# Kernel optimization log

Hardware: AMD Instinct MI355X
Metric: run time of the kernel (lower is better)

Reference implementation:

```python
import jax, jax.numpy as jnp
import numpy as np

N_NODES = 50000


def setup_inputs() -> dict:
    key = jax.random.key(0)
    ks = jax.random.split(key, 9)
    B, N, E, IN = 4, N_NODES, 800000, 32
    x = jax.random.normal(ks[0], (B, N, IN), dtype=jnp.float32)
    edge_index = jax.random.randint(ks[1], (2, E), 0, N, dtype=jnp.int64)
    edge_attr = jax.random.normal(ks[2], (E, 1), dtype=jnp.float32)
    W1 = jax.random.normal(ks[3], (2 * IN + 1, 32), dtype=jnp.float32) * 0.1
    b1 = jax.random.normal(ks[4], (32,), dtype=jnp.float32) * 0.1
    W2 = jax.random.normal(ks[5], (32, 30), dtype=jnp.float32) * 0.1
    b2 = jax.random.normal(ks[6], (30,), dtype=jnp.float32) * 0.1
    W3 = jax.random.normal(ks[7], (30, 32), dtype=jnp.float32) * 0.1
    b3 = jax.random.normal(ks[8], (32,), dtype=jnp.float32) * 0.1
    return {"x": x, "edge_index": edge_index, "edge_attr": edge_attr,
            "W1": W1, "b1": b1, "W2": W2, "b2": b2, "W3": W3, "b3": b3}


def reference(x, edge_index, edge_attr, W1, b1, W2, b2, W3, b3):
    B, N, _ = x.shape
    src, tgt = edge_index[0], edge_index[1]
    # normalize edge attributes over edges (torch .std uses ddof=1)
    ea = (edge_attr - edge_attr.mean(axis=0)) / edge_attr.std(axis=0, ddof=1)
    node_src = x[:, src]      # [B, E, in]
    node_tgt = x[:, tgt]      # [B, E, in]
    ea_b = jnp.broadcast_to(ea[None], (B,) + ea.shape)
    h = jnp.concatenate([node_src, node_tgt, ea_b], axis=-1)  # [B, E, 2*in+1]
    h = jax.nn.sigmoid(h @ W1 + b1)
    h = jax.nn.sigmoid(h @ W2 + b2)   # [B, E, 30]
    seg = lambda vals, idx: jax.ops.segment_sum(vals, idx, num_segments=N)
    out_add = jax.vmap(seg, in_axes=(0, None))(h, tgt)    # [B, N, 30]
    out_sub = jax.vmap(seg, in_axes=(0, None))(-h, src)   # [B, N, 30]
    out = out_add + out_sub
    return jax.nn.sigmoid(out @ W3 + b3)  # [B, N, out_dim]
```

## Files before the change

kernel.cpp:

```cpp
#include <hip/hip_runtime.h>
#include <math.h>

#define B_SZ 4
#define IN_F 32
#define H1_F 32
#define H2_F 30
#define TPW 16
#define HREP 16

typedef unsigned int uint;
typedef unsigned short ushort;
typedef __attribute__((ext_vector_type(8))) short bf16x8;
typedef __attribute__((ext_vector_type(4))) float f32x4;

__device__ __forceinline__ float fastrcp(float x) {
#if __has_builtin(__builtin_amdgcn_rcpf)
    return __builtin_amdgcn_rcpf(x);
#else
    return 1.f / x;
#endif
}
__device__ __forceinline__ float sigmoidf_(float x) {
    return fastrcp(1.f + __expf(-x));
}

__device__ __forceinline__ ushort f2bf(float f) {
    uint u = __float_as_uint(f);
    return (ushort)((u + 0x7FFFu + ((u >> 16) & 1u)) >> 16);
}
__device__ __forceinline__ float bf2f(ushort v) { return __uint_as_float(((uint)v) << 16); }
__device__ __forceinline__ uint pk2(float a, float b) {
    return (uint)f2bf(a) | ((uint)f2bf(b) << 16);
}

union Frag { bf16x8 v; ushort us[8]; uint u[4]; };

__global__ void __launch_bounds__(256) stats_xcvt_kernel(
    const float* __restrict__ ea, const int* __restrict__ ei,
    const float* __restrict__ x, float2* __restrict__ psums,
    int* __restrict__ cnt, ushort* __restrict__ xb,
    int E, int N, long long n8) {
    long long i = (long long)blockIdx.x * 256 + threadIdx.x;
    if (i < n8) {
        const float4* p = (const float4*)(x + i * 8);
        float4 v0 = p[0], v1 = p[1];
        uint4 o;
        o.x = pk2(v0.x, v0.y); o.y = pk2(v0.z, v0.w);
        o.z = pk2(v1.x, v1.y); o.w = pk2(v1.z, v1.w);
        *(uint4*)(xb + i * 8) = o;
    }
    int e = blockIdx.x * 256 + threadIdx.x;
    int* myc = cnt + (size_t)(blockIdx.x & (HREP - 1)) * N;
    float a = (e < E) ? ea[e] : 0.f;
    if (e < E) {
        atomicAdd(&myc[ei[E + e]], 1);
        atomicAdd(&myc[ei[e]], 1);
    }
    float v = a, v2 = a * a;
    for (int off = 32; off > 0; off >>= 1) {
        v  += __shfl_down(v, off);
        v2 += __shfl_down(v2, off);
    }
    __shared__ float s1[4], s2[4];
    int wid = threadIdx.x >> 6, lane = threadIdx.x & 63;
    if (lane == 0) { s1[wid] = v; s2[wid] = v2; }
    __syncthreads();
    if (threadIdx.x == 0) {
        float2 p;
        p.x = s1[0] + s1[1] + s1[2] + s1[3];
        p.y = s2[0] + s2[1] + s2[2] + s2[3];
        psums[blockIdx.x] = p;
    }
}

__global__ void __launch_bounds__(256) sums_reduce_kernel(
    const float2* __restrict__ psums, float* __restrict__ sums, int nblk) {
    float v = 0.f, v2 = 0.f;
    for (int i = threadIdx.x; i < nblk; i += 256) {
        float2 p = psums[i];
        v += p.x; v2 += p.y;
    }
    for (int off = 32; off > 0; off >>= 1) {
        v  += __shfl_down(v, off);
        v2 += __shfl_down(v2, off);
    }
    __shared__ float s1[4], s2[4];
    int wid = threadIdx.x >> 6, lane = threadIdx.x & 63;
    if (lane == 0) { s1[wid] = v; s2[wid] = v2; }
    __syncthreads();
    if (threadIdx.x == 0) {
        sums[0] = s1[0] + s1[1] + s1[2] + s1[3];
        sums[1] = s2[0] + s2[1] + s2[2] + s2[3];
    }
}

__global__ void __launch_bounds__(256) scan1_kernel(const int* __restrict__ cnt,
                                                    int* __restrict__ offs,
                                                    int* __restrict__ bsum, int n) {
    __shared__ int wtot[4];
    int base = blockIdx.x * 1024 + threadIdx.x * 4;
    int4 v = {0, 0, 0, 0};
    if (base + 3 < n) {
#pragma unroll
        for (int r = 0; r < HREP; r++) {
            int4 t = *(const int4*)(cnt + (size_t)r * n + base);
            v.x += t.x; v.y += t.y; v.z += t.z; v.w += t.w;
        }
    } else {
        for (int r = 0; r < HREP; r++) {
            const int* c = cnt + (size_t)r * n;
            if (base < n)     v.x += c[base];
            if (base + 1 < n) v.y += c[base + 1];
            if (base + 2 < n) v.z += c[base + 2];
            if (base + 3 < n) v.w += c[base + 3];
        }
    }
    int s = v.x + v.y + v.z + v.w;
    int incl = s;
    int lane = threadIdx.x & 63;
    for (int d = 1; d < 64; d <<= 1) {
        int t = __shfl_up(incl, d);
        if (lane >= d) incl += t;
    }
    int wid = threadIdx.x >> 6;
    if (lane == 63) wtot[wid] = incl;
    __syncthreads();
    int woff = 0, tot = 0;
#pragma unroll
    for (int w = 0; w < 4; w++) {
        int t = wtot[w];
        if (w < wid) woff += t;
        tot += t;
    }
    int excl = woff + incl - s;
    int4 o;
    o.x = excl; o.y = excl + v.x; o.z = o.y + v.y; o.w = o.z + v.z;
    if (base + 3 < n) *(int4*)(offs + base) = o;
    else {
        if (base < n)     offs[base] = o.x;
        if (base + 1 < n) offs[base + 1] = o.y;
        if (base + 2 < n) offs[base + 2] = o.z;
        if (base + 3 < n) offs[base + 3] = o.w;
    }
    if (threadIdx.x == 0) bsum[blockIdx.x] = tot;
}

__global__ void scan2_kernel(int* __restrict__ bsum, int* __restrict__ offs,
                             int nb, int n) {
    int lane = threadIdx.x;
    if (nb <= 64) {
        int v = (lane < nb) ? bsum[lane] : 0;
        int incl = v;
        for (int d = 1; d < 64; d <<= 1) {
            int t = __shfl_up(incl, d);
            if (lane >= d) incl += t;
        }
        if (lane < nb) bsum[lane] = incl - v;
        if (lane == 63) offs[n] = incl;
    } else if (lane == 0) {
        int run = 0;
        for (int i = 0; i < nb; i++) { int t = bsum[i]; bsum[i] = run; run += t; }
        offs[n] = run;
    }
}

__global__ void __launch_bounds__(256) scan3_kernel(int* __restrict__ offs,
                                                    int* __restrict__ cursor,
                                                    const int* __restrict__ bsum, int n) {
    int base = blockIdx.x * 1024 + threadIdx.x * 4;
    int add = bsum[blockIdx.x];
    if (base + 3 < n) {
        int4 v = *(const int4*)(offs + base);
        v.x += add; v.y += add; v.z += add; v.w += add;
        *(int4*)(offs + base) = v;
        *(int4*)(cursor + base) = v;
    } else {
        for (int k = 0; k < 4; k++) {
            int i = base + k;
            if (i < n) { int v = offs[i] + add; offs[i] = v; cursor[i] = v; }
        }
    }
}

__global__ void __launch_bounds__(256) edge_mlp_e4(
    const ushort* __restrict__ xb,
    const int* __restrict__ ei, const float* __restrict__ ea,
    const float* __restrict__ W1, const float* __restrict__ b1,
    const float* __restrict__ W2, const float* __restrict__ b2,
    const float* __restrict__ sums, int* __restrict__ cursor,
    int* __restrict__ list, ushort* __restrict__ h,
    int E, int N, int tiles) {
    __shared__ ushort __attribute__((aligned(16))) hbuf[4][16 * 40];
    int w = threadIdx.x >> 6;
    int lane = threadIdx.x & 63;
    int n16 = lane & 15;
    int q = lane >> 4;

    Frag w1f[2][2];
#pragma unroll
    for (int t = 0; t < 2; t++)
#pragma unroll
        for (int s = 0; s < 2; s++)
#pragma unroll
            for (int j = 0; j < 4; j++) {
                int k0 = 32 * s + q * 8 + 2 * j;
                w1f[t][s].u[j] = pk2(W1[(size_t)k0 * 32 + 16 * t + n16],
                                     W1[(size_t)(k0 + 1) * 32 + 16 * t + n16]);
            }
    Frag w2f[2];
#pragma unroll
    for (int t = 0; t < 2; t++) {
        int m = 16 * t + n16;
#pragma unroll
        for (int j = 0; j < 4; j++) {
            int k0 = q * 8 + 2 * j;
            float a = (m < H2_F) ? W2[(size_t)k0 * H2_F + m] : 0.f;
            float d = (m < H2_F) ? W2[(size_t)(k0 + 1) * H2_F + m] : 0.f;
            w2f[t].u[j] = pk2(a, d);
        }
    }
    float b1q[2][4], w1Lq[2][4], b2q[2][4];
#pragma unroll
    for (int t = 0; t < 2; t++)
#pragma unroll
        for (int r = 0; r < 4; r++) {
            int col = 16 * t + q * 4 + r;
            b1q[t][r]  = b1[col];
            w1Lq[t][r] = W1[(size_t)64 * 32 + col];
            b2q[t][r]  = (col < H2_F) ? b2[col] : 0.f;
        }

    float mean = sums[0] / (float)E;
    float var = (sums[1] - (float)E * mean * mean) / (float)(E - 1);
    float istd = rsqrtf(var);

    int b  = n16 & 3;
    int el = n16 >> 2;
    int gw = blockIdx.x * 4 + w;
    int tile0 = gw * TPW;
    if (tile0 >= tiles) return;

    int src, tgt; float eav; bool vrow; Frag a0, a1;
    {
        int eA = tile0 * 4 + el; vrow = eA < E; int c = vrow ? eA : E - 1;
        src = ei[c]; tgt = ei[E + c]; eav = (ea[c] - mean) * istd;
        *(uint4*)&a0.u[0] = *(const uint4*)(xb + ((size_t)b * N + src) * IN_F + q * 8);
        *(uint4*)&a1.u[0] = *(const uint4*)(xb + ((size_t)b * N + tgt) * IN_F + q * 8);
        if (lane < 8) {
            int eS = tile0 * 4 + (lane >> 1);
            if (eS < E) {
                int node = (lane & 1) ? ei[eS] : ei[E + eS];
                int s = atomicAdd(&cursor[node], 1);
                list[s] = eS | (int)(((uint)(lane & 1)) << 31);
            }
        }
    }

    for (int tix = 0; tix < TPW; ++tix) {
        int tile = tile0 + tix;
        if (tile >= tiles) break;

        int nsrc = 0, ntgt = 0; float neav = 0.f; bool nvrow = false;
        Frag na0, na1;
        na0.u[0] = na0.u[1] = na0.u[2] = na0.u[3] = 0; na1 = na0;
        bool hn = (tix + 1 < TPW) && (tile + 1 < tiles);
        if (hn) {
            int eA = (tile + 1) * 4 + el; nvrow = eA < E; int c = nvrow ? eA : E - 1;
            nsrc = ei[c]; ntgt = ei[E + c]; neav = (ea[c] - mean) * istd;
            *(uint4*)&na0.u[0] = *(const uint4*)(xb + ((size_t)b * N + nsrc) * IN_F + q * 8);
            *(uint4*)&na1.u[0] = *(const uint4*)(xb + ((size_t)b * N + ntgt) * IN_F + q * 8);
            if (lane < 8) {
                int eS = (tile + 1) * 4 + (lane >> 1);
                if (eS < E) {
                    int node = (lane & 1) ? ei[eS] : ei[E + eS];
                    int s = atomicAdd(&cursor[node], 1);
                    list[s] = eS | (int)(((uint)(lane & 1)) << 31);
                }
            }
        }

        f32x4 acc0, acc1;
#pragma unroll
        for (int r = 0; r < 4; r++) {
            acc0[r] = b1q[0][r] + eav * w1Lq[0][r];
            acc1[r] = b1q[1][r] + eav * w1Lq[1][r];
        }
        acc0 = __builtin_amdgcn_mfma_f32_16x16x32_bf16(w1f[0][0].v, a0.v, acc0, 0, 0, 0);
        acc0 = __builtin_amdgcn_mfma_f32_16x16x32_bf16(w1f[0][1].v, a1.v, acc0, 0, 0, 0);
        acc1 = __builtin_amdgcn_mfma_f32_16x16x32_bf16(w1f[1][0].v, a0.v, acc1, 0, 0, 0);
        acc1 = __builtin_amdgcn_mfma_f32_16x16x32_bf16(w1f[1][1].v, a1.v, acc1, 0, 0, 0);

        uint u0 = pk2(sigmoidf_(acc0[0]), sigmoidf_(acc0[1]));
        uint u1 = pk2(sigmoidf_(acc0[2]), sigmoidf_(acc0[3]));
        uint u2 = pk2(sigmoidf_(acc1[0]), sigmoidf_(acc1[1]));
        uint u3 = pk2(sigmoidf_(acc1[2]), sigmoidf_(acc1[3]));
        uint2 p01 = {u0, u1}, p23 = {u2, u3};
        *(uint2*)&hbuf[w][n16 * 40 + q * 4]      = p01;
        *(uint2*)&hbuf[w][n16 * 40 + 16 + q * 4] = p23;

        Frag ha;
        *(uint4*)&ha.u[0] = *(const uint4*)&hbuf[w][n16 * 40 + q * 8];

        f32x4 c0, c1;
#pragma unroll
        for (int r = 0; r < 4; r++) { c0[r] = b2q[0][r]; c1[r] = b2q[1][r]; }
        c0 = __builtin_amdgcn_mfma_f32_16x16x32_bf16(w2f[0].v, ha.v, c0, 0, 0, 0);
        c1 = __builtin_amdgcn_mfma_f32_16x16x32_bf16(w2f[1].v, ha.v, c1, 0, 0, 0);

        uint g0 = pk2(sigmoidf_(c0[0]), sigmoidf_(c0[1]));
        uint g1 = pk2(sigmoidf_(c0[2]), sigmoidf_(c0[3]));
        uint g2 = pk2(sigmoidf_(c1[0]), sigmoidf_(c1[1]));
        uint g3 = pk2(sigmoidf_(c1[2]), sigmoidf_(c1[3]));

        if (vrow) {
            uint* bt = (uint*)h + (size_t)(tile * 4 + el) * 64 + b * 16;
            uint2 t01; t01.x = g0; t01.y = g1;
            uint2 t23; t23.x = g2; t23.y = g3;
            *(uint2*)(bt + q * 2)     = t01;
            *(uint2*)(bt + 8 + q * 2) = t23;
        }

        src = nsrc; tgt = ntgt; eav = neav; vrow = nvrow;
        a0 = na0; a1 = na1;
    }
}

__global__ void __launch_bounds__(256) gather_e4(
    const ushort* __restrict__ h, const int* __restrict__ list,
    const int* __restrict__ offs, const float* __restrict__ W3,
    const float* __restrict__ b3, float* __restrict__ out, int N) {
    __shared__ float sW3[H2_F * 32];
    __shared__ float sb3[32];
    __shared__ float sacc[4][B_SZ][H2_F];
    for (int i = threadIdx.x; i < H2_F * 32; i += 256) sW3[i] = W3[i];
    if (threadIdx.x < 32) sb3[threadIdx.x] = b3[threadIdx.x];
    __syncthreads();

    int w = threadIdx.x >> 6, lane = threadIdx.x & 63;
    int n = blockIdx.x * 4 + w;
    if (n >= N) return;

    int s = offs[n], e = offs[n + 1];
    int r = (lane < 60) ? lane : 0;
    int bq = r / 15, jp = r % 15;
    const uint* h32 = (const uint*)h;
    float a0 = 0.f, a1 = 0.f;
    int i = (lane < 60) ? s : e;
    for (; i + 3 < e; i += 4) {
        int v0 = list[i], v1 = list[i + 1], v2 = list[i + 2], v3 = list[i + 3];
        uint d0 = h32[(size_t)(v0 & 0x7FFFFFFF) * 64 + bq * 16 + jp];
        uint d1 = h32[(size_t)(v1 & 0x7FFFFFFF) * 64 + bq * 16 + jp];
        uint d2 = h32[(size_t)(v2 & 0x7FFFFFFF) * 64 + bq * 16 + jp];
        uint d3 = h32[(size_t)(v3 & 0x7FFFFFFF) * 64 + bq * 16 + jp];
        float g0 = (v0 < 0) ? -1.f : 1.f;
        float g1 = (v1 < 0) ? -1.f : 1.f;
        float g2 = (v2 < 0) ? -1.f : 1.f;
        float g3 = (v3 < 0) ? -1.f : 1.f;
        a0 += g0 * bf2f((ushort)d0) + g1 * bf2f((ushort)d1)
            + g2 * bf2f((ushort)d2) + g3 * bf2f((ushort)d3);
        a1 += g0 * bf2f((ushort)(d0 >> 16)) + g1 * bf2f((ushort)(d1 >> 16))
            + g2 * bf2f((ushort)(d2 >> 16)) + g3 * bf2f((ushort)(d3 >> 16));
    }
    for (; i < e; i++) {
        int v = list[i];
        uint d = h32[(size_t)(v & 0x7FFFFFFF) * 64 + bq * 16 + jp];
        float g = (v < 0) ? -1.f : 1.f;
        a0 += g * bf2f((ushort)d);
        a1 += g * bf2f((ushort)(d >> 16));
    }
    if (lane < 60) {
        sacc[w][bq][jp * 2]     = a0;
        sacc[w][bq][jp * 2 + 1] = a1;
    }
    int b = lane >> 4, k = lane & 15;
    float o0 = sb3[k], o1 = sb3[k + 16];
#pragma unroll
    for (int j = 0; j < H2_F; j++) {
        float v = sacc[w][b][j];
        o0 += v * sW3[j * 32 + k];
        o1 += v * sW3[j * 32 + k + 16];
    }
    float* op = out + ((size_t)b * N + n) * 32;
    op[k]      = sigmoidf_(o0);
    op[k + 16] = sigmoidf_(o1);
}

__global__ void __launch_bounds__(256) scatter_kernel(const int* __restrict__ ei,
                                                      int* __restrict__ cursor,
                                                      int* __restrict__ list, int E, int N) {
    int e = blockIdx.x * 256 + threadIdx.x;
    if (e < E) {
        int tgt = ei[E + e];
        int p = atomicAdd(&cursor[tgt], 1);
        list[p] = e;
        int src = ei[e];
        int q = atomicAdd(&cursor[src], 1);
        list[q] = e | (int)0x80000000u;
    }
}

template<bool USE_XB>
__global__ void __launch_bounds__(256) edge_mlp_mfma2(
    const float* __restrict__ x, const ushort* __restrict__ xb,
    const int* __restrict__ ei, const float* __restrict__ ea,
    const float* __restrict__ W1, const float* __restrict__ b1,
    const float* __restrict__ W2, const float* __restrict__ b2,
    const float* __restrict__ sums, ushort* __restrict__ h,
    int E, int N, int tiles) {
    __shared__ ushort __attribute__((aligned(16))) hbuf[4][16 * 40];
    int w = threadIdx.x >> 6;
    int lane = threadIdx.x & 63;
    int n16 = lane & 15;
    int q = lane >> 4;

    Frag w1f[2][2];
#pragma unroll
    for (int t = 0; t < 2; t++)
#pragma unroll
        for (int s = 0; s < 2; s++)
#pragma unroll
            for (int j = 0; j < 4; j++) {
                int k0 = 32 * s + q * 8 + 2 * j;
                w1f[t][s].u[j] = pk2(W1[(size_t)k0 * 32 + 16 * t + n16],
                                     W1[(size_t)(k0 + 1) * 32 + 16 * t + n16]);
            }
    Frag w2f[2];
#pragma unroll
    for (int t = 0; t < 2; t++) {
        int m = 16 * t + n16;
#pragma unroll
        for (int j = 0; j < 4; j++) {
            int k0 = q * 8 + 2 * j;
            float a = (m < H2_F) ? W2[(size_t)k0 * H2_F + m] : 0.f;
            float d = (m < H2_F) ? W2[(size_t)(k0 + 1) * H2_F + m] : 0.f;
            w2f[t].u[j] = pk2(a, d);
        }
    }
    float b1q[2][4], w1Lq[2][4], b2q[2][4];
#pragma unroll
    for (int t = 0; t < 2; t++)
#pragma unroll
        for (int r = 0; r < 4; r++) {
            int col = 16 * t + q * 4 + r;
            b1q[t][r]  = b1[col];
            w1Lq[t][r] = W1[(size_t)64 * 32 + col];
            b2q[t][r]  = (col < H2_F) ? b2[col] : 0.f;
        }

    float mean = sums[0] / (float)E;
    float var = (sums[1] - (float)E * mean * mean) / (float)(E - 1);
    float istd = rsqrtf(var);

    int b = n16 & 3;
    int eoff = n16 >> 2;
    int gw = blockIdx.x * 4 + w;

    for (int tix = 0; tix < TPW; ++tix) {
        int tile = gw * TPW + tix;
        if (tile >= tiles) break;
        int e0 = tile * 4;
        int eA = e0 + eoff;
        bool vrow = eA < E;
        int eAc = vrow ? eA : E - 1;
        int src = ei[eAc], tgt = ei[E + eAc];
        float eav = (ea[eAc] - mean) * istd;

        Frag a0, a1;
        if (USE_XB) {
            *(uint4*)&a0.u[0] = *(const uint4*)(xb + ((size_t)b * N + src) * IN_F + q * 8);
            *(uint4*)&a1.u[0] = *(const uint4*)(xb + ((size_t)b * N + tgt) * IN_F + q * 8);
        } else {
            const float4* ps = (const float4*)(x + ((size_t)b * N + src) * IN_F + q * 8);
            float4 s0 = ps[0], s1 = ps[1];
            const float4* pt = (const float4*)(x + ((size_t)b * N + tgt) * IN_F + q * 8);
            float4 t0 = pt[0], t1 = pt[1];
            a0.u[0] = pk2(s0.x, s0.y); a0.u[1] = pk2(s0.z, s0.w);
            a0.u[2] = pk2(s1.x, s1.y); a0.u[3] = pk2(s1.z, s1.w);
            a1.u[0] = pk2(t0.x, t0.y); a1.u[1] = pk2(t0.z, t0.w);
            a1.u[2] = pk2(t1.x, t1.y); a1.u[3] = pk2(t1.z, t1.w);
        }

        f32x4 acc0, acc1;
#pragma unroll
        for (int r = 0; r < 4; r++) {
            acc0[r] = b1q[0][r] + eav * w1Lq[0][r];
            acc1[r] = b1q[1][r] + eav * w1Lq[1][r];
        }
        acc0 = __builtin_amdgcn_mfma_f32_16x16x32_bf16(w1f[0][0].v, a0.v, acc0, 0, 0, 0);
        acc0 = __builtin_amdgcn_mfma_f32_16x16x32_bf16(w1f[0][1].v, a1.v, acc0, 0, 0, 0);
        acc1 = __builtin_amdgcn_mfma_f32_16x16x32_bf16(w1f[1][0].v, a0.v, acc1, 0, 0, 0);
        acc1 = __builtin_amdgcn_mfma_f32_16x16x32_bf16(w1f[1][1].v, a1.v, acc1, 0, 0, 0);

        uint u0 = pk2(sigmoidf_(acc0[0]), sigmoidf_(acc0[1]));
        uint u1 = pk2(sigmoidf_(acc0[2]), sigmoidf_(acc0[3]));
        uint u2 = pk2(sigmoidf_(acc1[0]), sigmoidf_(acc1[1]));
        uint u3 = pk2(sigmoidf_(acc1[2]), sigmoidf_(acc1[3]));
        uint2 p01 = {u0, u1}, p23 = {u2, u3};
        *(uint2*)&hbuf[w][n16 * 40 + q * 4]      = p01;
        *(uint2*)&hbuf[w][n16 * 40 + 16 + q * 4] = p23;

        Frag ha;
        *(uint4*)&ha.u[0] = *(const uint4*)&hbuf[w][n16 * 40 + q * 8];

        f32x4 c0, c1;
#pragma unroll
        for (int r = 0; r < 4; r++) { c0[r] = b2q[0][r]; c1[r] = b2q[1][r]; }
        c0 = __builtin_amdgcn_mfma_f32_16x16x32_bf16(w2f[0].v, ha.v, c0, 0, 0, 0);
        c1 = __builtin_amdgcn_mfma_f32_16x16x32_bf16(w2f[1].v, ha.v, c1, 0, 0, 0);

        uint g0 = pk2(sigmoidf_(c0[0]), sigmoidf_(c0[1]));
        uint g1 = pk2(sigmoidf_(c0[2]), sigmoidf_(c0[3]));
        uint g2 = pk2(sigmoidf_(c1[0]), sigmoidf_(c1[1]));
        uint g3 = pk2(sigmoidf_(c1[2]), sigmoidf_(c1[3]));
        if (vrow) {
            uint* base = (uint*)(h + (size_t)(e0 * 4 + n16) * H2_F);
            base[q * 2]     = g0;
            base[q * 2 + 1] = g1;
            base[8 + q * 2] = g2;
            if (q < 3) base[8 + q * 2 + 1] = g3;
        }
    }
}

__global__ void __launch_bounds__(256) gather_final(
    const ushort* __restrict__ h, const int* __restrict__ list,
    const int* __restrict__ offs, const float* __restrict__ W3,
    const float* __restrict__ b3, float* __restrict__ out, int N) {
    __shared__ float sW3[H2_F * 32];
    __shared__ float sb3[32];
    __shared__ float sacc[4][B_SZ][H2_F];
    for (int i = threadIdx.x; i < H2_F * 32; i += 256) sW3[i] = W3[i];
    if (threadIdx.x < 32) sb3[threadIdx.x] = b3[threadIdx.x];
    __syncthreads();

    int w = threadIdx.x >> 6, lane = threadIdx.x & 63;
    int n = blockIdx.x * 4 + w;
    if (n >= N) return;

    if (lane < 60) {
        int bq = lane / 15, jp = lane % 15;
        float a0 = 0.f, a1 = 0.f;
        int s = offs[n], e = offs[n + 1];
        int i = s;
        for (; i + 4 <= e; i += 4) {
            int v0 = list[i], v1 = list[i + 1], v2 = list[i + 2], v3 = list[i + 3];
            uint d0 = *(const uint*)(h + (size_t)(v0 & 0x7FFFFFFF) * 120 + bq * 30 + jp * 2);
            uint d1 = *(const uint*)(h + (size_t)(v1 & 0x7FFFFFFF) * 120 + bq * 30 + jp * 2);
            uint d2 = *(const uint*)(h + (size_t)(v2 & 0x7FFFFFFF) * 120 + bq * 30 + jp * 2);
            uint d3 = *(const uint*)(h + (size_t)(v3 & 0x7FFFFFFF) * 120 + bq * 30 + jp * 2);
            float g0 = (v0 < 0) ? -1.f : 1.f;
            float g1 = (v1 < 0) ? -1.f : 1.f;
            float g2 = (v2 < 0) ? -1.f : 1.f;
            float g3 = (v3 < 0) ? -1.f : 1.f;
            a0 += g0 * bf2f((ushort)d0) + g1 * bf2f((ushort)d1)
                + g2 * bf2f((ushort)d2) + g3 * bf2f((ushort)d3);
            a1 += g0 * bf2f((ushort)(d0 >> 16)) + g1 * bf2f((ushort)(d1 >> 16))
                + g2 * bf2f((ushort)(d2 >> 16)) + g3 * bf2f((ushort)(d3 >> 16));
        }
        for (; i < e; i++) {
            int v = list[i];
            uint d = *(const uint*)(h + (size_t)(v & 0x7FFFFFFF) * 120 + bq * 30 + jp * 2);
            float g = (v < 0) ? -1.f : 1.f;
            a0 += g * bf2f((ushort)d);
            a1 += g * bf2f((ushort)(d >> 16));
        }
        sacc[w][bq][jp * 2]     = a0;
        sacc[w][bq][jp * 2 + 1] = a1;
    }
    int b = lane >> 4, k = lane & 15;
    float o0 = sb3[k], o1 = sb3[k + 16];
#pragma unroll
    for (int j = 0; j < H2_F; j++) {
        float v = sacc[w][b][j];
        o0 += v * sW3[j * 32 + k];
        o1 += v * sW3[j * 32 + k + 16];
    }
    float* op = out + ((size_t)b * N + n) * 32;
    op[k]      = sigmoidf_(o0);
    op[k + 16] = sigmoidf_(o1);
}

extern "C" void kernel_launch(void* const* d_in, const int* in_sizes, int n_in,
                              void* d_out, int out_size, void* d_ws, size_t ws_size,
                              hipStream_t stream) {
    const float* x  = (const float*)d_in[0];
    const int*   ei = (const int*)d_in[1];
    const float* ea = (const float*)d_in[2];
    const float* W1 = (const float*)d_in[3];
    const float* b1 = (const float*)d_in[4];
    const float* W2 = (const float*)d_in[5];
    const float* b2 = (const float*)d_in[6];
    const float* W3 = (const float*)d_in[7];
    const float* b3 = (const float*)d_in[8];
    float* out = (float*)d_out;

    const int E  = in_sizes[2];
    const int N  = in_sizes[0] / (B_SZ * IN_F);
    const int BN = B_SZ * N;
    const int nb = (N + 1023) / 1024;
    const long long n8 = (long long)BN * IN_F / 8;
    const int nblkC = (int)(((long long)E > n8 ? (long long)E : n8) + 255) / 256;

    char* base = (char*)d_ws;

    size_t off = 0;
    int* cnt    = (int*)(base + off); off += (size_t)HREP * N * 4;
    float* sums = (float*)(base + off); off += 8;
    int* offs   = (int*)(base + off); off += (size_t)(N + 1) * 4;
    int* cursor = (int*)(base + off); off += (size_t)N * 4;
    int* bsum   = (int*)(base + off); off += 4096;
    off = (off + 255) & ~(size_t)255;
    float2* psums = (float2*)(base + off); off += (size_t)nblkC * 8;
    off = (off + 255) & ~(size_t)255;
    int* list   = (int*)(base + off); off += (size_t)2 * E * 4;
    off = (off + 255) & ~(size_t)255;
    ushort* h   = (ushort*)(base + off); off += (size_t)E * 256;
    off = (off + 255) & ~(size_t)255;
    ushort* xb  = (ushort*)(base + off); off += (size_t)BN * IN_F * 2;
    size_t needA = off;

    size_t offB = 0;
    int* cntB    = (int*)(base + offB); offB += (size_t)HREP * N * 4;
    float* sumsB = (float*)(base + offB); offB += 8;
    int* offsB   = (int*)(base + offB); offB += (size_t)(N + 1) * 4;
    int* cursorB = (int*)(base + offB); offB += (size_t)N * 4;
    int* bsumB   = (int*)(base + offB); offB += 4096;
    offB = (offB + 255) & ~(size_t)255;
    float2* psumsB = (float2*)(base + offB); offB += (size_t)nblkC * 8;
    int* listB   = (int*)(base + offB); offB += (size_t)2 * E * 4;
    offB = (offB + 255) & ~(size_t)255;
    ushort* hB   = (ushort*)(base + offB); offB += (size_t)E * 240;
    offB = (offB + 255) & ~(size_t)255;
    ushort* xbB  = (ushort*)(base + offB);
    size_t needB = offB + (size_t)BN * IN_F * 2;

    if (ws_size >= needA) {
        const int tiles = (E + 3) / 4;
        const int waves = (tiles + TPW - 1) / TPW;
        const int eblocks = (waves + 3) / 4;
        hipMemsetAsync(cnt, 0, (size_t)HREP * N * 4 + 8, stream);
        stats_xcvt_kernel<<<nblkC, 256, 0, stream>>>(ea, ei, x, psums, cnt, xb, E, N, n8);
        sums_reduce_kernel<<<1, 256, 0, stream>>>(psums, sums, nblkC);
        scan1_kernel<<<nb, 256, 0, stream>>>(cnt, offs, bsum, N);
        scan2_kernel<<<1, 64, 0, stream>>>(bsum, offs, nb, N);
        scan3_kernel<<<nb, 256, 0, stream>>>(offs, cursor, bsum, N);
        edge_mlp_e4<<<eblocks, 256, 0, stream>>>(xb, ei, ea, W1, b1, W2, b2,
                                                 sums, cursor, list, h, E, N, tiles);
        gather_e4<<<(N + 3) / 4, 256, 0, stream>>>(h, list, offs, W3, b3, out, N);
    } else {
        const int tiles = (E + 3) / 4;
        const int waves = (tiles + TPW - 1) / TPW;
        const int eblocks = (waves + 3) / 4;
        bool use_xb = (ws_size >= needB);
        hipMemsetAsync(cntB, 0, (size_t)HREP * N * 4 + 8, stream);
        stats_xcvt_kernel<<<nblkC, 256, 0, stream>>>(ea, ei, x, psumsB, cntB,
                                                     use_xb ? xbB : (ushort*)nullptr,
                                                     E, N, use_xb ? n8 : 0LL);
        sums_reduce_kernel<<<1, 256, 0, stream>>>(psumsB, sumsB, nblkC);
        scan1_kernel<<<nb, 256, 0, stream>>>(cntB, offsB, bsumB, N);
        scan2_kernel<<<1, 64, 0, stream>>>(bsumB, offsB, nb, N);
        scan3_kernel<<<nb, 256, 0, stream>>>(offsB, cursorB, bsumB, N);
        scatter_kernel<<<(E + 255) / 256, 256, 0, stream>>>(ei, cursorB, listB, E, N);
        if (use_xb)
            edge_mlp_mfma2<true><<<eblocks, 256, 0, stream>>>(x, xbB, ei, ea, W1, b1,
                                                              W2, b2, sumsB, hB, E, N, tiles);
        else
            edge_mlp_mfma2<false><<<eblocks, 256, 0, stream>>>(x, xbB, ei, ea, W1, b1,
                                                               W2, b2, sumsB, hB, E, N, tiles);
        gather_final<<<(N + 3) / 4, 256, 0, stream>>>(hB, listB, offsB, W3, b3, out, N);
    }
}
```

Baseline: 438.3 us.

## Use hardware bf16 pack, nontemporal list stores, and 8-way gather unroll

```diff
diff --git a/kernel.cpp b/kernel.cpp
--- a/kernel.cpp
+++ b/kernel.cpp
@@ -10,6 +10,7 @@
 
 typedef unsigned int uint;
 typedef unsigned short ushort;
+typedef unsigned long long ull;
 typedef __attribute__((ext_vector_type(8))) short bf16x8;
 typedef __attribute__((ext_vector_type(4))) float f32x4;
 
@@ -31,6 +32,11 @@
 __device__ __forceinline__ float bf2f(ushort v) { return __uint_as_float(((uint)v) << 16); }
 __device__ __forceinline__ uint pk2(float a, float b) {
     return (uint)f2bf(a) | ((uint)f2bf(b) << 16);
+}
+__device__ __forceinline__ uint pk2f(float a, float b) {
+    uint r;
+    asm("v_cvt_pk_bf16_f32 %0, %1, %2" : "=v"(r) : "v"(a), "v"(b));
+    return r;
 }
 
 union Frag { bf16x8 v; ushort us[8]; uint u[4]; };
@@ -45,8 +51,8 @@
         const float4* p = (const float4*)(x + i * 8);
         float4 v0 = p[0], v1 = p[1];
         uint4 o;
-        o.x = pk2(v0.x, v0.y); o.y = pk2(v0.z, v0.w);
-        o.z = pk2(v1.x, v1.y); o.w = pk2(v1.z, v1.w);
+        o.x = pk2f(v0.x, v0.y); o.y = pk2f(v0.z, v0.w);
+        o.z = pk2f(v1.x, v1.y); o.w = pk2f(v1.z, v1.w);
         *(uint4*)(xb + i * 8) = o;
     }
     int e = blockIdx.x * 256 + threadIdx.x;
@@ -251,7 +257,7 @@
             if (eS < E) {
                 int node = (lane & 1) ? ei[eS] : ei[E + eS];
                 int s = atomicAdd(&cursor[node], 1);
-                list[s] = eS | (int)(((uint)(lane & 1)) << 31);
+                __builtin_nontemporal_store(eS | (int)(((uint)(lane & 1)) << 31), &list[s]);
             }
         }
     }
@@ -274,7 +280,7 @@
                 if (eS < E) {
                     int node = (lane & 1) ? ei[eS] : ei[E + eS];
                     int s = atomicAdd(&cursor[node], 1);
-                    list[s] = eS | (int)(((uint)(lane & 1)) << 31);
+                    __builtin_nontemporal_store(eS | (int)(((uint)(lane & 1)) << 31), &list[s]);
                 }
             }
         }
@@ -290,10 +296,10 @@
         acc1 = __builtin_amdgcn_mfma_f32_16x16x32_bf16(w1f[1][0].v, a0.v, acc1, 0, 0, 0);
         acc1 = __builtin_amdgcn_mfma_f32_16x16x32_bf16(w1f[1][1].v, a1.v, acc1, 0, 0, 0);
 
-        uint u0 = pk2(sigmoidf_(acc0[0]), sigmoidf_(acc0[1]));
-        uint u1 = pk2(sigmoidf_(acc0[2]), sigmoidf_(acc0[3]));
-        uint u2 = pk2(sigmoidf_(acc1[0]), sigmoidf_(acc1[1]));
-        uint u3 = pk2(sigmoidf_(acc1[2]), sigmoidf_(acc1[3]));
+        uint u0 = pk2f(sigmoidf_(acc0[0]), sigmoidf_(acc0[1]));
+        uint u1 = pk2f(sigmoidf_(acc0[2]), sigmoidf_(acc0[3]));
+        uint u2 = pk2f(sigmoidf_(acc1[0]), sigmoidf_(acc1[1]));
+        uint u3 = pk2f(sigmoidf_(acc1[2]), sigmoidf_(acc1[3]));
         uint2 p01 = {u0, u1}, p23 = {u2, u3};
         *(uint2*)&hbuf[w][n16 * 40 + q * 4]      = p01;
         *(uint2*)&hbuf[w][n16 * 40 + 16 + q * 4] = p23;
@@ -307,10 +313,10 @@
         c0 = __builtin_amdgcn_mfma_f32_16x16x32_bf16(w2f[0].v, ha.v, c0, 0, 0, 0);
         c1 = __builtin_amdgcn_mfma_f32_16x16x32_bf16(w2f[1].v, ha.v, c1, 0, 0, 0);
 
-        uint g0 = pk2(sigmoidf_(c0[0]), sigmoidf_(c0[1]));
-        uint g1 = pk2(sigmoidf_(c0[2]), sigmoidf_(c0[3]));
-        uint g2 = pk2(sigmoidf_(c1[0]), sigmoidf_(c1[1]));
-        uint g3 = pk2(sigmoidf_(c1[2]), sigmoidf_(c1[3]));
+        uint g0 = pk2f(sigmoidf_(c0[0]), sigmoidf_(c0[1]));
+        uint g1 = pk2f(sigmoidf_(c0[2]), sigmoidf_(c0[3]));
+        uint g2 = pk2f(sigmoidf_(c1[0]), sigmoidf_(c1[1]));
+        uint g3 = pk2f(sigmoidf_(c1[2]), sigmoidf_(c1[3]));
 
         if (vrow) {
             uint* bt = (uint*)h + (size_t)(tile * 4 + el) * 64 + b * 16;
@@ -346,6 +352,30 @@
     const uint* h32 = (const uint*)h;
     float a0 = 0.f, a1 = 0.f;
     int i = (lane < 60) ? s : e;
+    for (; i + 7 < e; i += 8) {
+        int v0 = list[i],     v1 = list[i + 1], v2 = list[i + 2], v3 = list[i + 3];
+        int v4 = list[i + 4], v5 = list[i + 5], v6 = list[i + 6], v7 = list[i + 7];
+        uint d0 = h32[(size_t)(v0 & 0x7FFFFFFF) * 64 + bq * 16 + jp];
+        uint d1 = h32[(size_t)(v1 & 0x7FFFFFFF) * 64 + bq * 16 + jp];
+        uint d2 = h32[(size_t)(v2 & 0x7FFFFFFF) * 64 + bq * 16 + jp];
+        uint d3 = h32[(size_t)(v3 & 0x7FFFFFFF) * 64 + bq * 16 + jp];
+        uint d4 = h32[(size_t)(v4 & 0x7FFFFFFF) * 64 + bq * 16 + jp];
+        uint d5 = h32[(size_t)(v5 & 0x7FFFFFFF) * 64 + bq * 16 + jp];
+        uint d6 = h32[(size_t)(v6 & 0x7FFFFFFF) * 64 + bq * 16 + jp];
+        uint d7 = h32[(size_t)(v7 & 0x7FFFFFFF) * 64 + bq * 16 + jp];
+        float g0 = (v0 < 0) ? -1.f : 1.f, g1 = (v1 < 0) ? -1.f : 1.f;
+        float g2 = (v2 < 0) ? -1.f : 1.f, g3 = (v3 < 0) ? -1.f : 1.f;
+        float g4 = (v4 < 0) ? -1.f : 1.f, g5 = (v5 < 0) ? -1.f : 1.f;
+        float g6 = (v6 < 0) ? -1.f : 1.f, g7 = (v7 < 0) ? -1.f : 1.f;
+        a0 += g0 * bf2f((ushort)d0) + g1 * bf2f((ushort)d1)
+            + g2 * bf2f((ushort)d2) + g3 * bf2f((ushort)d3)
+            + g4 * bf2f((ushort)d4) + g5 * bf2f((ushort)d5)
+            + g6 * bf2f((ushort)d6) + g7 * bf2f((ushort)d7);
+        a1 += g0 * bf2f((ushort)(d0 >> 16)) + g1 * bf2f((ushort)(d1 >> 16))
+            + g2 * bf2f((ushort)(d2 >> 16)) + g3 * bf2f((ushort)(d3 >> 16))
+            + g4 * bf2f((ushort)(d4 >> 16)) + g5 * bf2f((ushort)(d5 >> 16))
+            + g6 * bf2f((ushort)(d6 >> 16)) + g7 * bf2f((ushort)(d7 >> 16));
+    }
     for (; i + 3 < e; i += 4) {
         int v0 = list[i], v1 = list[i + 1], v2 = list[i + 2], v3 = list[i + 3];
         uint d0 = h32[(size_t)(v0 & 0x7FFFFFFF) * 64 + bq * 16 + jp];
```

Result: no change. 434.0 us (-1.0%).
